# Optimization experiments

Hardware: AMD Instinct MI355X
Metric: run time of the kernel (lower is better)

The kernel has to match this reference:

```python
import jax, jax.numpy as jnp
import numpy as np

S = 128           # seq_len
B = 256           # input_bits (bits per token, also neurons per head)
H = 16            # num_heads
NB = 12           # n_bits_per_neuron -> LUT size 2^12
PB = 7            # relative-position bits = ceil(log2(max_seq_len))
HEAD_IN = 2 * B + PB   # concat(query, key, rel_pos_bits) = 519
THRESH = H // 2


def setup_inputs() -> dict:
    key = jax.random.key(0)
    k1, k2, k3 = jax.random.split(key, 3)
    tokens = jax.random.randint(k1, (S, B), 0, 2, dtype=jnp.int32)           # binary token bits
    memory = jax.random.normal(k2, (H, B, 2 ** NB), dtype=jnp.float32)       # RAM LUT contents per head/neuron
    connections = jax.random.randint(k3, (H, B, NB), 0, HEAD_IN, dtype=jnp.int32)  # per-neuron input-bit wiring
    return {"tokens": tokens, "memory": memory, "connections": connections}


def reference(tokens, memory, connections):
    idx = jnp.arange(S)
    rel = idx[:, None] - idx[None, :]                         # [S,S] i - j
    mask = (rel >= 0).astype(jnp.int32)                        # causal mask (j <= i)
    relc = jnp.clip(rel, 0, S - 1)
    # relative-distance binary encoding, LSB first: [S,S,PB]
    pos_bits = ((relc[..., None] >> jnp.arange(PB)) & 1).astype(jnp.int32)
    q = jnp.broadcast_to(tokens[:, None, :], (S, S, B))
    k = jnp.broadcast_to(tokens[None, :, :], (S, S, B))
    head_in = jnp.concatenate([q, k, pos_bits], axis=-1)       # [S,S,HEAD_IN]
    # RAM address per (query i, key j, head h, neuron n): pack NB wired bits, LSB first
    addr = jnp.zeros((S, S, H, B), dtype=jnp.int32)
    for b in range(NB):  # tiny fixed loop over bit planes, fully vectorized over S,S,H,B
        addr = addr + (head_in[..., connections[:, :, b]] << b)
    # LUT gather: memory[h, n, addr] -> [S,S,H,B]
    h_idx = jnp.arange(H)[:, None]
    n_idx = jnp.arange(B)[None, :]
    vals = memory[h_idx, n_idx, addr]
    bits = (vals > 0.0).astype(jnp.int32)                      # RAM neuron output bit
    # XOR accumulation over attended keys == masked sum mod 2: [S,H,B]
    head_res = jnp.sum(bits * mask[:, :, None, None], axis=1) % 2
    # majority vote across heads per bit
    ones_count = jnp.sum(head_res, axis=1)                     # [S,B]
    return (ones_count > THRESH).astype(jnp.int32)
```

## Files before the change

kernel.cpp:

```cpp
#include <hip/hip_runtime.h>
#include <hip/hip_bf16.h>


#define S 128
#define B 256
#define H 16
#define NB 12

__global__ __launch_bounds__(1024) void softram_kernel(
    const int* __restrict__ tokens,
    const float* __restrict__ memory,
    const int* __restrict__ connections,
    int* __restrict__ out)
{
    const int n = blockIdx.x;
    const int tid = threadIdx.x;

    __shared__ unsigned int   lut[H][128];
    __shared__ unsigned int   tok[S][8];
    __shared__ unsigned short aqs[H][S];
    __shared__ unsigned short aks[H][S];
    __shared__ unsigned short aps[H][S];
    __shared__ int            conns[H][NB];
    __shared__ unsigned short partial[H][S];

    #pragma unroll
    for (int q = 0; q < 2; ++q) {
        int s = tid + (q << 10);
        int h = s >> 7;
        int d = s & 127;
        const float4* mrow = (const float4*)(memory + (((size_t)((h << 8) | n)) << 12));
        unsigned int w = 0;
        #pragma unroll
        for (int t = 0; t < 8; ++t) {
            float4 v = mrow[(d << 3) + t];
            w |= (unsigned int)(v.x > 0.f) << (4 * t + 0);
            w |= (unsigned int)(v.y > 0.f) << (4 * t + 1);
            w |= (unsigned int)(v.z > 0.f) << (4 * t + 2);
            w |= (unsigned int)(v.w > 0.f) << (4 * t + 3);
        }
        lut[h][d] = w;
    }

    {
        int i = tid >> 3;
        int w = tid & 7;
        const int4* tp = (const int4*)tokens;
        unsigned int v = 0;
        #pragma unroll
        for (int t = 0; t < 8; ++t) {
            int4 x = tp[i * 64 + w * 8 + t];
            v |= (unsigned int)(x.x & 1) << (4 * t + 0);
            v |= (unsigned int)(x.y & 1) << (4 * t + 1);
            v |= (unsigned int)(x.z & 1) << (4 * t + 2);
            v |= (unsigned int)(x.w & 1) << (4 * t + 3);
        }
        tok[i][w] = v;
    }

    if (tid < H * NB) {
        int h = tid / NB;
        int b = tid - h * NB;
        conns[h][b] = connections[h * (B * NB) + n * NB + b];
    }

    __syncthreads();

    #pragma unroll
    for (int q = 0; q < 2; ++q) {
        int e = tid + (q << 10);
        int h = e >> 7;
        int ii = e & 127;
        unsigned int aq = 0, ak = 0, ap = 0;
        #pragma unroll
        for (int b = 0; b < NB; ++b) {
            int c = conns[h][b];
            if (c < 256) {
                aq |= ((tok[ii][c >> 5] >> (c & 31)) & 1u) << b;
            } else if (c < 512) {
                int c2 = c - 256;
                ak |= ((tok[ii][c2 >> 5] >> (c2 & 31)) & 1u) << b;
            } else {
                ap |= (unsigned int)((ii >> (c - 512)) & 1) << b;
            }
        }
        aqs[h][ii] = (unsigned short)aq;
        aks[h][ii] = (unsigned short)ak;
        aps[h][ii] = (unsigned short)ap;
    }

    __syncthreads();

    const int h    = tid >> 6;
    const int lane = tid & 63;
    const int i0 = lane;
    const int i1 = 127 - lane;

    const unsigned int aq0 = aqs[h][i0];
    const unsigned int aq1 = aqs[h][i1];
    const unsigned short* __restrict__ akrow = &aks[h][0];
    const unsigned short* __restrict__ aprow = &aps[h][0];
    const unsigned int* __restrict__ lrow = &lut[h][0];
    unsigned int p0 = 0, p1 = 0;
    #pragma unroll 8
    for (int k = 0; k <= 128; ++k) {
        bool first = (k <= lane);
        int j   = first ? k : (k - lane - 1);
        int imj = first ? (lane - k) : (128 - k);
        unsigned int aqv = first ? aq0 : aq1;
        unsigned int addr = aqv | (unsigned int)akrow[j] | (unsigned int)aprow[imj];
        unsigned int bit = (lrow[addr >> 5] >> (addr & 31)) & 1u;
        p0 ^= first ? bit : 0u;
        p1 ^= first ? 0u : bit;
    }
    partial[h][i0] = (unsigned short)p0;
    partial[h][i1] = (unsigned short)p1;

    __syncthreads();

    if (tid < S) {
        int tot = 0;
        #pragma unroll
        for (int hh = 0; hh < H; ++hh) tot += partial[hh][tid];
        out[tid * B + n] = (tot > (H / 2)) ? 1 : 0;
    }
}

extern "C" void kernel_launch(void* const* d_in, const int* in_sizes, int n_in,
                              void* d_out, int out_size, void* d_ws, size_t ws_size,
                              hipStream_t stream) {
    const int*   tokens      = (const int*)d_in[0];
    const float* memory      = (const float*)d_in[1];
    const int*   connections = (const int*)d_in[2];
    int*         out         = (int*)d_out;
    (void)in_sizes; (void)n_in; (void)out_size; (void)d_ws; (void)ws_size;

    softram_kernel<<<B, 1024, 0, stream>>>(tokens, memory, connections, out);
}
```

Before: 118.8 us.

## Split work across head-pair blocks with separate token-pack and reduce kernels

The single 256-block kernel of 1024 threads becomes three kernels. A one-block kernel packs the token bits into workspace. The main kernel runs 2048 blocks of 256 threads, each handling one neuron and a pair of heads, with keys split between two waves by parity. Per-block head counts go to a byte workspace, and a final kernel sums them and applies the majority threshold. The aim is better occupancy and load balance, and to stop every block repacking the tokens. The cost is two extra launches and a workspace round trip.

```diff
diff --git a/kernel.cpp b/kernel.cpp
--- a/kernel.cpp
+++ b/kernel.cpp
@@ -7,123 +7,142 @@
 #define H 16
 #define NB 12
 
-__global__ __launch_bounds__(1024) void softram_kernel(
-    const int* __restrict__ tokens,
+__global__ __launch_bounds__(256) void softram_pack(
+    const int* __restrict__ tokens, unsigned int* __restrict__ ws_tok)
+{
+    const int tid = threadIdx.x;
+    const int4* tp = (const int4*)tokens;
+    #pragma unroll
+    for (int q = 0; q < 4; ++q) {
+        int e = tid + (q << 8);
+        int i = e >> 3, w = e & 7;
+        unsigned int v = 0;
+        #pragma unroll
+        for (int u = 0; u < 8; ++u) {
+            int4 x = tp[i * 64 + w * 8 + u];
+            v |= (unsigned int)(x.x & 1) << (4 * u + 0);
+            v |= (unsigned int)(x.y & 1) << (4 * u + 1);
+            v |= (unsigned int)(x.z & 1) << (4 * u + 2);
+            v |= (unsigned int)(x.w & 1) << (4 * u + 3);
+        }
+        ws_tok[e] = v;
+    }
+}
+
+__global__ __launch_bounds__(256, 8) void softram_main(
     const float* __restrict__ memory,
     const int* __restrict__ connections,
-    int* __restrict__ out)
+    const unsigned int* __restrict__ ws_tok,
+    unsigned char* __restrict__ ws_cnt)
 {
-    const int n = blockIdx.x;
+    const int bx  = blockIdx.x;
+    const int n   = bx & 255;
+    const int hp  = bx >> 8;
     const int tid = threadIdx.x;
 
-    __shared__ unsigned int   lut[H][128];
-    __shared__ unsigned int   tok[S][8];
-    __shared__ unsigned short aqs[H][S];
-    __shared__ unsigned short aks[H][S];
-    __shared__ unsigned short aps[H][S];
-    __shared__ int            conns[H][NB];
-    __shared__ unsigned short partial[H][S];
+    __shared__ unsigned int   lut[2][128];
+    __shared__ unsigned int   tok[S * 8];
+    __shared__ unsigned short aqs[2][S], aks[2][S], aps[2][S];
+    __shared__ int            conns[2][NB];
+    __shared__ unsigned short partial[2][2][S];
+
+    {
+        int hh = tid >> 7, d = tid & 127;
+        const float4* mrow =
+            (const float4*)(memory + ((size_t)((((hp << 1) | hh) << 8) | n) << 12));
+        unsigned int w = 0;
+        #pragma unroll
+        for (int u = 0; u < 8; ++u) {
+            float4 v = mrow[(d << 3) + u];
+            w |= (unsigned int)(v.x > 0.f) << (4 * u + 0);
+            w |= (unsigned int)(v.y > 0.f) << (4 * u + 1);
+            w |= (unsigned int)(v.z > 0.f) << (4 * u + 2);
+            w |= (unsigned int)(v.w > 0.f) << (4 * u + 3);
+        }
+        lut[hh][d] = w;
+    }
 
     #pragma unroll
-    for (int q = 0; q < 2; ++q) {
-        int s = tid + (q << 10);
-        int h = s >> 7;
-        int d = s & 127;
-        const float4* mrow = (const float4*)(memory + (((size_t)((h << 8) | n)) << 12));
-        unsigned int w = 0;
-        #pragma unroll
-        for (int t = 0; t < 8; ++t) {
-            float4 v = mrow[(d << 3) + t];
-            w |= (unsigned int)(v.x > 0.f) << (4 * t + 0);
-            w |= (unsigned int)(v.y > 0.f) << (4 * t + 1);
-            w |= (unsigned int)(v.z > 0.f) << (4 * t + 2);
-            w |= (unsigned int)(v.w > 0.f) << (4 * t + 3);
-        }
-        lut[h][d] = w;
-    }
+    for (int q = 0; q < 4; ++q)
+        tok[tid + (q << 8)] = ws_tok[tid + (q << 8)];
 
-    {
-        int i = tid >> 3;
-        int w = tid & 7;
-        const int4* tp = (const int4*)tokens;
-        unsigned int v = 0;
-        #pragma unroll
-        for (int t = 0; t < 8; ++t) {
-            int4 x = tp[i * 64 + w * 8 + t];
-            v |= (unsigned int)(x.x & 1) << (4 * t + 0);
-            v |= (unsigned int)(x.y & 1) << (4 * t + 1);
-            v |= (unsigned int)(x.z & 1) << (4 * t + 2);
-            v |= (unsigned int)(x.w & 1) << (4 * t + 3);
-        }
-        tok[i][w] = v;
-    }
-
-    if (tid < H * NB) {
-        int h = tid / NB;
-        int b = tid - h * NB;
-        conns[h][b] = connections[h * (B * NB) + n * NB + b];
+    if (tid < 2 * NB) {
+        int hh = tid / NB, b = tid - hh * NB;
+        conns[hh][b] = connections[((hp << 1) | hh) * (B * NB) + n * NB + b];
     }
 
     __syncthreads();
 
-    #pragma unroll
-    for (int q = 0; q < 2; ++q) {
-        int e = tid + (q << 10);
-        int h = e >> 7;
-        int ii = e & 127;
+    {
+        int hh = tid >> 7, ii = tid & 127;
         unsigned int aq = 0, ak = 0, ap = 0;
         #pragma unroll
         for (int b = 0; b < NB; ++b) {
-            int c = conns[h][b];
+            int c = conns[hh][b];
             if (c < 256) {
-                aq |= ((tok[ii][c >> 5] >> (c & 31)) & 1u) << b;
+                aq |= ((tok[ii * 8 + (c >> 5)] >> (c & 31)) & 1u) << b;
             } else if (c < 512) {
                 int c2 = c - 256;
-                ak |= ((tok[ii][c2 >> 5] >> (c2 & 31)) & 1u) << b;
+                ak |= ((tok[ii * 8 + (c2 >> 5)] >> (c2 & 31)) & 1u) << b;
             } else {
                 ap |= (unsigned int)((ii >> (c - 512)) & 1) << b;
             }
         }
-        aqs[h][ii] = (unsigned short)aq;
-        aks[h][ii] = (unsigned short)ak;
-        aps[h][ii] = (unsigned short)ap;
+        aqs[hh][ii] = (unsigned short)aq;
+        aks[hh][ii] = (unsigned short)ak;
+        aps[hh][ii] = (unsigned short)ap;
     }
 
     __syncthreads();
 
-    const int h    = tid >> 6;
-    const int lane = tid & 63;
-    const int i0 = lane;
-    const int i1 = 127 - lane;
+    const int wave = tid >> 6, lane = tid & 63;
+    const int hh = wave >> 1, r = wave & 1;
+    const int i0 = lane, i1 = 127 - lane;
+    const int c0 = (lane - r >= 0) ? (((lane - r) >> 1) + 1) : 0;
+    const int ctot = 65 - r;
 
-    const unsigned int aq0 = aqs[h][i0];
-    const unsigned int aq1 = aqs[h][i1];
-    const unsigned short* __restrict__ akrow = &aks[h][0];
-    const unsigned short* __restrict__ aprow = &aps[h][0];
-    const unsigned int* __restrict__ lrow = &lut[h][0];
+    const unsigned int aq0 = aqs[hh][i0];
+    const unsigned int aq1 = aqs[hh][i1];
+    const unsigned short* __restrict__ akrow = &aks[hh][0];
+    const unsigned short* __restrict__ aprow = &aps[hh][0];
+    const unsigned int* __restrict__ lrow = &lut[hh][0];
+
     unsigned int p0 = 0, p1 = 0;
     #pragma unroll 8
-    for (int k = 0; k <= 128; ++k) {
-        bool first = (k <= lane);
-        int j   = first ? k : (k - lane - 1);
-        int imj = first ? (lane - k) : (128 - k);
+    for (int k = 0; k < ctot; ++k) {
+        bool first = (k < c0);
+        int jf = r + 2 * k;
+        int j  = first ? jf : (jf - 2 * c0);
+        int ii = first ? i0 : i1;
+        int imj = ii - j;
         unsigned int aqv = first ? aq0 : aq1;
         unsigned int addr = aqv | (unsigned int)akrow[j] | (unsigned int)aprow[imj];
         unsigned int bit = (lrow[addr >> 5] >> (addr & 31)) & 1u;
         p0 ^= first ? bit : 0u;
         p1 ^= first ? 0u : bit;
     }
-    partial[h][i0] = (unsigned short)p0;
-    partial[h][i1] = (unsigned short)p1;
+    partial[hh][r][i0] = (unsigned short)p0;
+    partial[hh][r][i1] = (unsigned short)p1;
 
     __syncthreads();
 
     if (tid < S) {
-        int tot = 0;
-        #pragma unroll
-        for (int hh = 0; hh < H; ++hh) tot += partial[hh][tid];
-        out[tid * B + n] = (tot > (H / 2)) ? 1 : 0;
+        int cnt = (partial[0][0][tid] ^ partial[0][1][tid])
+                + (partial[1][0][tid] ^ partial[1][1][tid]);
+        ws_cnt[(hp * 256 + n) * 128 + tid] = (unsigned char)cnt;
     }
+}
+
+__global__ __launch_bounds__(256) void softram_reduce(
+    const unsigned char* __restrict__ ws_cnt, int* __restrict__ out)
+{
+    const int i = blockIdx.x;
+    const int n = threadIdx.x;
+    int tot = 0;
+    #pragma unroll
+    for (int hp = 0; hp < 8; ++hp)
+        tot += ws_cnt[(hp * 256 + n) * 128 + i];
+    out[i * B + n] = (tot > (H / 2)) ? 1 : 0;
 }
 
 extern "C" void kernel_launch(void* const* d_in, const int* in_sizes, int n_in,
@@ -133,7 +152,12 @@
     const float* memory      = (const float*)d_in[1];
     const int*   connections = (const int*)d_in[2];
     int*         out         = (int*)d_out;
-    (void)in_sizes; (void)n_in; (void)out_size; (void)d_ws; (void)ws_size;
+    (void)in_sizes; (void)n_in; (void)out_size; (void)ws_size;
 
-    softram_kernel<<<B, 1024, 0, stream>>>(tokens, memory, connections, out);
+    unsigned int*  ws_tok = (unsigned int*)d_ws;
+    unsigned char* ws_cnt = (unsigned char*)d_ws + 4096;
+
+    softram_pack<<<1, 256, 0, stream>>>(tokens, ws_tok);
+    softram_main<<<8 * B, 256, 0, stream>>>(memory, connections, ws_tok, ws_cnt);
+    softram_reduce<<<S, 256, 0, stream>>>(ws_cnt, out);
 }
```

Measured after the change: 134.9 us. 1.14x slower.

## Byte-per-entry LUT in two head halves with prefetch overlapping lookup phase

Applied to the files above, without the earlier changes.

The packed-bit LUT is replaced by a one-byte-per-entry LUT in shared memory. Half the heads (8) are processed at a time, and the second half's memory rows are prefetched into registers while the first half's lookups run. Each head is now split across two waves by key residue mod 4, and each wave handles two residues, so the work per wave and the loop trip count are rebalanced. This removes the shift/mask bit extraction and spreads latency, at the cost of more registers (16 float4 held), an extra phase with syncs, and a launch_bounds occupancy hint.

```diff
diff --git a/kernel.cpp b/kernel.cpp
--- a/kernel.cpp
+++ b/kernel.cpp
@@ -7,7 +7,7 @@
 #define H 16
 #define NB 12
 
-__global__ __launch_bounds__(1024) void softram_kernel(
+__global__ __launch_bounds__(1024, 4) void softram_kernel(
     const int* __restrict__ tokens,
     const float* __restrict__ memory,
     const int* __restrict__ connections,
@@ -16,70 +16,64 @@
     const int n = blockIdx.x;
     const int tid = threadIdx.x;
 
-    __shared__ unsigned int   lut[H][128];
-    __shared__ unsigned int   tok[S][8];
-    __shared__ unsigned short aqs[H][S];
+    __shared__ unsigned char  lutb[8 * 4096];
+    __shared__ unsigned int   tok[S * 8];
     __shared__ unsigned short aks[H][S];
     __shared__ unsigned short aps[H][S];
+    __shared__ unsigned short aqs[H][S];
     __shared__ int            conns[H][NB];
-    __shared__ unsigned short partial[H][S];
-
-    #pragma unroll
-    for (int q = 0; q < 2; ++q) {
-        int s = tid + (q << 10);
-        int h = s >> 7;
-        int d = s & 127;
-        const float4* mrow = (const float4*)(memory + (((size_t)((h << 8) | n)) << 12));
-        unsigned int w = 0;
-        #pragma unroll
-        for (int t = 0; t < 8; ++t) {
-            float4 v = mrow[(d << 3) + t];
-            w |= (unsigned int)(v.x > 0.f) << (4 * t + 0);
-            w |= (unsigned int)(v.y > 0.f) << (4 * t + 1);
-            w |= (unsigned int)(v.z > 0.f) << (4 * t + 2);
-            w |= (unsigned int)(v.w > 0.f) << (4 * t + 3);
-        }
-        lut[h][d] = w;
-    }
+    __shared__ unsigned char  parts[H][2][S];
 
     {
-        int i = tid >> 3;
-        int w = tid & 7;
-        const int4* tp = (const int4*)tokens;
-        unsigned int v = 0;
+        float4 v[8];
         #pragma unroll
-        for (int t = 0; t < 8; ++t) {
-            int4 x = tp[i * 64 + w * 8 + t];
-            v |= (unsigned int)(x.x & 1) << (4 * t + 0);
-            v |= (unsigned int)(x.y & 1) << (4 * t + 1);
-            v |= (unsigned int)(x.z & 1) << (4 * t + 2);
-            v |= (unsigned int)(x.w & 1) << (4 * t + 3);
+        for (int q = 0; q < 8; ++q) {
+            const float4* mrow = (const float4*)(memory + ((size_t)((q << 8) | n) << 12));
+            v[q] = mrow[tid];
         }
-        tok[i][w] = v;
+        {
+            int i = tid >> 3, w = tid & 7;
+            const int4* tp = (const int4*)tokens;
+            unsigned int t = 0;
+            #pragma unroll
+            for (int u = 0; u < 8; ++u) {
+                int4 x = tp[i * 64 + w * 8 + u];
+                t |= (unsigned int)(x.x & 1) << (4 * u + 0);
+                t |= (unsigned int)(x.y & 1) << (4 * u + 1);
+                t |= (unsigned int)(x.z & 1) << (4 * u + 2);
+                t |= (unsigned int)(x.w & 1) << (4 * u + 3);
+            }
+            tok[tid] = t;
+        }
+        if (tid < H * NB) {
+            int h = tid / NB, b = tid - h * NB;
+            conns[h][b] = connections[h * (B * NB) + n * NB + b];
+        }
+        unsigned int* lw = (unsigned int*)lutb;
+        #pragma unroll
+        for (int q = 0; q < 8; ++q) {
+            unsigned int w = (unsigned int)(v[q].x > 0.f)
+                           | ((unsigned int)(v[q].y > 0.f) << 8)
+                           | ((unsigned int)(v[q].z > 0.f) << 16)
+                           | ((unsigned int)(v[q].w > 0.f) << 24);
+            lw[(q << 10) + tid] = w;
+        }
     }
-
-    if (tid < H * NB) {
-        int h = tid / NB;
-        int b = tid - h * NB;
-        conns[h][b] = connections[h * (B * NB) + n * NB + b];
-    }
-
     __syncthreads();
 
     #pragma unroll
-    for (int q = 0; q < 2; ++q) {
-        int e = tid + (q << 10);
-        int h = e >> 7;
-        int ii = e & 127;
+    for (int e0 = 0; e0 < 2; ++e0) {
+        int e = tid + (e0 << 10);
+        int h = e >> 7, ii = e & 127;
         unsigned int aq = 0, ak = 0, ap = 0;
         #pragma unroll
         for (int b = 0; b < NB; ++b) {
             int c = conns[h][b];
             if (c < 256) {
-                aq |= ((tok[ii][c >> 5] >> (c & 31)) & 1u) << b;
+                aq |= ((tok[ii * 8 + (c >> 5)] >> (c & 31)) & 1u) << b;
             } else if (c < 512) {
                 int c2 = c - 256;
-                ak |= ((tok[ii][c2 >> 5] >> (c2 & 31)) & 1u) << b;
+                ak |= ((tok[ii * 8 + (c2 >> 5)] >> (c2 & 31)) & 1u) << b;
             } else {
                 ap |= (unsigned int)((ii >> (c - 512)) & 1) << b;
             }
@@ -88,40 +82,83 @@
         aks[h][ii] = (unsigned short)ak;
         aps[h][ii] = (unsigned short)ap;
     }
-
     __syncthreads();
 
-    const int h    = tid >> 6;
-    const int lane = tid & 63;
-    const int i0 = lane;
-    const int i1 = 127 - lane;
+    const int wave = tid >> 6, lane = tid & 63;
+    const int hl = wave >> 1;
+    const int r2 = wave & 1;
+    const int i0 = lane, i1 = 127 - lane;
 
-    const unsigned int aq0 = aqs[h][i0];
-    const unsigned int aq1 = aqs[h][i1];
-    const unsigned short* __restrict__ akrow = &aks[h][0];
-    const unsigned short* __restrict__ aprow = &aps[h][0];
-    const unsigned int* __restrict__ lrow = &lut[h][0];
-    unsigned int p0 = 0, p1 = 0;
-    #pragma unroll 8
-    for (int k = 0; k <= 128; ++k) {
-        bool first = (k <= lane);
-        int j   = first ? k : (k - lane - 1);
-        int imj = first ? (lane - k) : (128 - k);
-        unsigned int aqv = first ? aq0 : aq1;
-        unsigned int addr = aqv | (unsigned int)akrow[j] | (unsigned int)aprow[imj];
-        unsigned int bit = (lrow[addr >> 5] >> (addr & 31)) & 1u;
-        p0 ^= first ? bit : 0u;
-        p1 ^= first ? 0u : bit;
+    float4 pre[8];
+    #pragma unroll
+    for (int q = 0; q < 8; ++q) {
+        const float4* mrow = (const float4*)(memory + ((size_t)(((8 + q) << 8) | n) << 12));
+        pre[q] = mrow[tid];
     }
-    partial[h][i0] = (unsigned short)p0;
-    partial[h][i1] = (unsigned short)p1;
 
+    auto phaseD = [&](int h) {
+        const unsigned int aq0 = aqs[h][i0];
+        const unsigned int aq1 = aqs[h][i1];
+        const unsigned short* __restrict__ akrow = &aks[h][0];
+        const unsigned short* __restrict__ aprow = &aps[h][0];
+        const unsigned char*  __restrict__ lrow  = &lutb[hl << 12];
+        int c0a[2], cta[2], c04a[2];
+        #pragma unroll
+        for (int s = 0; s < 2; ++s) {
+            int r  = r2 + 2 * s;
+            int c0 = (i0 >= r) ? (((i0 - r) >> 2) + 1) : 0;
+            int c1 = ((i1 - r) >> 2) + 1;
+            c0a[s] = c0; cta[s] = c0 + c1; c04a[s] = c0 << 2;
+        }
+        unsigned int acc = 0;
+        #pragma unroll 11
+        for (int k = 0; k < 33; ++k) {
+            #pragma unroll
+            for (int s = 0; s < 2; ++s) {
+                const int r = r2 + 2 * s;
+                bool first = k < c0a[s];
+                bool valid = k < cta[s];
+                int jb  = r + 4 * k;
+                int j   = first ? jb : (jb - c04a[s]);
+                int ii  = first ? i0 : i1;
+                int imj = (ii - j) & 255;
+                unsigned int aqv  = first ? aq0 : aq1;
+                unsigned int akv  = akrow[j];
+                unsigned int apv  = aprow[imj];
+                unsigned int addr = (aqv | akv | apv) & 4095;
+                unsigned int bit  = lrow[addr];
+                unsigned int contrib = bit << (first ? 0 : 16);
+                acc ^= valid ? contrib : 0u;
+            }
+        }
+        parts[h][r2][i0] = (unsigned char)(acc & 1u);
+        parts[h][r2][i1] = (unsigned char)((acc >> 16) & 1u);
+    };
+
+    phaseD(hl);
+    __syncthreads();
+
+    {
+        unsigned int* lw = (unsigned int*)lutb;
+        #pragma unroll
+        for (int q = 0; q < 8; ++q) {
+            unsigned int w = (unsigned int)(pre[q].x > 0.f)
+                           | ((unsigned int)(pre[q].y > 0.f) << 8)
+                           | ((unsigned int)(pre[q].z > 0.f) << 16)
+                           | ((unsigned int)(pre[q].w > 0.f) << 24);
+            lw[(q << 10) + tid] = w;
+        }
+    }
+    __syncthreads();
+
+    phaseD(8 + hl);
     __syncthreads();
 
     if (tid < S) {
         int tot = 0;
         #pragma unroll
-        for (int hh = 0; hh < H; ++hh) tot += partial[hh][tid];
+        for (int h = 0; h < H; ++h)
+            tot += parts[h][0][tid] ^ parts[h][1][tid];
         out[tid * B + n] = (tot > (H / 2)) ? 1 : 0;
     }
 }
```

Measured after the change: 149.5 us. 25.9% more time.

## Double-buffer LUT loads via async global-to-LDS and pipeline per head pair

Applied to the files above, without the earlier changes.

Memory LUT rows are streamed two heads at a time into a double-buffered LDS staging area with global_load_lds async copies, overlapping the next pair's load with the current pair's lookup loop. The LUT is stored as one byte per entry rather than bit-packed words, removing the shift/mask on each lookup. Key positions are split across 8 waves per head with strided residues, and partial XORs are reduced through LDS each round. This costs more LDS and a barrier pair per round. It also relies on the async copies being complete by the barrier.

```diff
diff --git a/kernel.cpp b/kernel.cpp
--- a/kernel.cpp
+++ b/kernel.cpp
@@ -7,121 +7,153 @@
 #define H 16
 #define NB 12
 
+typedef __attribute__((address_space(3))) void       lds_void;
+typedef const __attribute__((address_space(1))) void glb_void;
+
+__device__ __forceinline__ void async16(const float* g, float* l) {
+    __builtin_amdgcn_global_load_lds((glb_void*)g, (lds_void*)l, 16, 0, 0);
+}
+
 __global__ __launch_bounds__(1024) void softram_kernel(
     const int* __restrict__ tokens,
     const float* __restrict__ memory,
     const int* __restrict__ connections,
     int* __restrict__ out)
 {
-    const int n = blockIdx.x;
-    const int tid = threadIdx.x;
+    const int n    = blockIdx.x;
+    const int tid  = threadIdx.x;
+    const int wv   = tid >> 6;
+    const int lane = tid & 63;
 
-    __shared__ unsigned int   lut[H][128];
-    __shared__ unsigned int   tok[S][8];
-    __shared__ unsigned short aqs[H][S];
+    __shared__ float          raw[2][8192];
+    __shared__ unsigned char  lutb[8192];
+    __shared__ unsigned int   tok[S * 8];
     __shared__ unsigned short aks[H][S];
     __shared__ unsigned short aps[H][S];
+    __shared__ unsigned short aqs[H][S];
     __shared__ int            conns[H][NB];
-    __shared__ unsigned short partial[H][S];
+    __shared__ unsigned char  parts_r[2][S][8];
+    __shared__ unsigned char  parts_all[S][H];
+
+    auto issue_round = [&](int r, int buf) {
+        #pragma unroll
+        for (int q = 0; q < 2; ++q) {
+            int c = wv * 2 + q;
+            int h = 2 * r + (c >> 4);
+            const float* g = memory + ((size_t)(h * 256 + n) << 12)
+                           + ((c & 15) << 8) + (lane << 2);
+            float* l = &raw[buf][c << 8];
+            async16(g, l);
+        }
+    };
+
+    auto pack_round = [&](int buf) {
+        const float4* rp = (const float4*)&raw[buf][0];
+        float4 a = rp[2 * tid], b4 = rp[2 * tid + 1];
+        unsigned w0 = (unsigned)(a.x > 0.f)        | ((unsigned)(a.y > 0.f) << 8)
+                    | ((unsigned)(a.z > 0.f) << 16)| ((unsigned)(a.w > 0.f) << 24);
+        unsigned w1 = (unsigned)(b4.x > 0.f)       | ((unsigned)(b4.y > 0.f) << 8)
+                    | ((unsigned)(b4.z > 0.f) << 16)|((unsigned)(b4.w > 0.f) << 24);
+        ((uint2*)lutb)[tid] = make_uint2(w0, w1);
+    };
+
+    issue_round(0, 0);
+    {
+        int i = tid >> 3, w = tid & 7;
+        const int4* tp = (const int4*)tokens;
+        unsigned int t = 0;
+        #pragma unroll
+        for (int u = 0; u < 8; ++u) {
+            int4 x = tp[i * 64 + w * 8 + u];
+            t |= (unsigned)(x.x & 1) << (4 * u + 0);
+            t |= (unsigned)(x.y & 1) << (4 * u + 1);
+            t |= (unsigned)(x.z & 1) << (4 * u + 2);
+            t |= (unsigned)(x.w & 1) << (4 * u + 3);
+        }
+        tok[tid] = t;
+    }
+    if (tid < H * NB) {
+        int h = tid / NB, b = tid - h * NB;
+        conns[h][b] = connections[h * (B * NB) + n * NB + b];
+    }
+    __syncthreads();
+
+    issue_round(1, 1);
 
     #pragma unroll
-    for (int q = 0; q < 2; ++q) {
-        int s = tid + (q << 10);
-        int h = s >> 7;
-        int d = s & 127;
-        const float4* mrow = (const float4*)(memory + (((size_t)((h << 8) | n)) << 12));
-        unsigned int w = 0;
-        #pragma unroll
-        for (int t = 0; t < 8; ++t) {
-            float4 v = mrow[(d << 3) + t];
-            w |= (unsigned int)(v.x > 0.f) << (4 * t + 0);
-            w |= (unsigned int)(v.y > 0.f) << (4 * t + 1);
-            w |= (unsigned int)(v.z > 0.f) << (4 * t + 2);
-            w |= (unsigned int)(v.w > 0.f) << (4 * t + 3);
-        }
-        lut[h][d] = w;
-    }
-
-    {
-        int i = tid >> 3;
-        int w = tid & 7;
-        const int4* tp = (const int4*)tokens;
-        unsigned int v = 0;
-        #pragma unroll
-        for (int t = 0; t < 8; ++t) {
-            int4 x = tp[i * 64 + w * 8 + t];
-            v |= (unsigned int)(x.x & 1) << (4 * t + 0);
-            v |= (unsigned int)(x.y & 1) << (4 * t + 1);
-            v |= (unsigned int)(x.z & 1) << (4 * t + 2);
-            v |= (unsigned int)(x.w & 1) << (4 * t + 3);
-        }
-        tok[i][w] = v;
-    }
-
-    if (tid < H * NB) {
-        int h = tid / NB;
-        int b = tid - h * NB;
-        conns[h][b] = connections[h * (B * NB) + n * NB + b];
-    }
-
-    __syncthreads();
-
-    #pragma unroll
-    for (int q = 0; q < 2; ++q) {
-        int e = tid + (q << 10);
-        int h = e >> 7;
-        int ii = e & 127;
-        unsigned int aq = 0, ak = 0, ap = 0;
+    for (int e0 = 0; e0 < 2; ++e0) {
+        int e = tid + (e0 << 10);
+        int h = e >> 7, ii = e & 127;
+        unsigned aq = 0, ak = 0, ap = 0;
         #pragma unroll
         for (int b = 0; b < NB; ++b) {
             int c = conns[h][b];
             if (c < 256) {
-                aq |= ((tok[ii][c >> 5] >> (c & 31)) & 1u) << b;
+                aq |= ((tok[ii * 8 + (c >> 5)] >> (c & 31)) & 1u) << b;
             } else if (c < 512) {
                 int c2 = c - 256;
-                ak |= ((tok[ii][c2 >> 5] >> (c2 & 31)) & 1u) << b;
+                ak |= ((tok[ii * 8 + (c2 >> 5)] >> (c2 & 31)) & 1u) << b;
             } else {
-                ap |= (unsigned int)((ii >> (c - 512)) & 1) << b;
+                ap |= (unsigned)((ii >> (c - 512)) & 1) << b;
             }
         }
         aqs[h][ii] = (unsigned short)aq;
         aks[h][ii] = (unsigned short)ak;
         aps[h][ii] = (unsigned short)ap;
     }
-
+    pack_round(0);
     __syncthreads();
 
-    const int h    = tid >> 6;
-    const int lane = tid & 63;
-    const int i0 = lane;
-    const int i1 = 127 - lane;
+    const int hh  = wv >> 3;
+    const int res = wv & 7;
+    const int i0 = lane, i1 = 127 - lane;
+    const int c0 = (i0 >= res) ? (((i0 - res) >> 3) + 1) : 0;
+    const int ct = c0 + (((i1 - res) >> 3) + 1);
+    const unsigned char* __restrict__ lrow = &lutb[hh << 12];
 
-    const unsigned int aq0 = aqs[h][i0];
-    const unsigned int aq1 = aqs[h][i1];
-    const unsigned short* __restrict__ akrow = &aks[h][0];
-    const unsigned short* __restrict__ aprow = &aps[h][0];
-    const unsigned int* __restrict__ lrow = &lut[h][0];
-    unsigned int p0 = 0, p1 = 0;
-    #pragma unroll 8
-    for (int k = 0; k <= 128; ++k) {
-        bool first = (k <= lane);
-        int j   = first ? k : (k - lane - 1);
-        int imj = first ? (lane - k) : (128 - k);
-        unsigned int aqv = first ? aq0 : aq1;
-        unsigned int addr = aqv | (unsigned int)akrow[j] | (unsigned int)aprow[imj];
-        unsigned int bit = (lrow[addr >> 5] >> (addr & 31)) & 1u;
-        p0 ^= first ? bit : 0u;
-        p1 ^= first ? 0u : bit;
+    for (int r = 0; r < 8; ++r) {
+        if (r < 6) issue_round(r + 2, r & 1);
+
+        const int h = 2 * r + hh;
+        const unsigned aq0 = aqs[h][i0], aq1 = aqs[h][i1];
+        const unsigned short* __restrict__ akr = &aks[h][0];
+        const unsigned short* __restrict__ apr = &aps[h][0];
+        unsigned accA = 0, accB = 0;
+        #pragma unroll
+        for (int k = 0; k < 17; ++k) {
+            bool first = (k < c0);
+            int j   = res + ((first ? k : (k - c0)) << 3);
+            int ii  = first ? i0 : i1;
+            int imj = (ii - j) & 127;
+            j &= 127;
+            unsigned addr = (first ? aq0 : aq1) | akr[j] | apr[imj];
+            unsigned v  = lrow[addr & 4095];
+            unsigned vv = (k < ct) ? v : 0u;
+            accA ^= first ? vv : 0u;
+            accB ^= first ? 0u : vv;
+        }
+        parts_r[hh][i0][res] = (unsigned char)(accA & 1u);
+        parts_r[hh][i1][res] = (unsigned char)(accB & 1u);
+
+        __syncthreads();
+
+        if (tid < 2 * S) {
+            int ph = tid >> 7, i = tid & 127;
+            uint2 pw = ((const uint2*)&parts_r[ph][i][0])[0];
+            unsigned x = pw.x ^ pw.y;
+            x ^= x >> 16; x ^= x >> 8;
+            parts_all[i][2 * r + ph] = (unsigned char)(x & 1u);
+        }
+        if (r < 7) pack_round((r + 1) & 1);
+
+        __syncthreads();
     }
-    partial[h][i0] = (unsigned short)p0;
-    partial[h][i1] = (unsigned short)p1;
-
-    __syncthreads();
 
     if (tid < S) {
+        const unsigned char* pa = &parts_all[tid][0];
         int tot = 0;
         #pragma unroll
-        for (int hh = 0; hh < H; ++hh) tot += partial[hh][tid];
+        for (int h2 = 0; h2 < H; ++h2) tot += pa[h2];
         out[tid * B + n] = (tot > (H / 2)) ? 1 : 0;
     }
 }
```

Measured after the change: 114.3 us. -3.7%, faster.
